# Kernel tuning notes

Hardware: AMD Instinct MI355X
Metric: run time of the kernel (lower is better)

## Reference

```python
import jax, jax.numpy as jnp
import numpy as np

N_NODES = 100000
N_EDGES = 3200000
D_IN = 256
D_OUT = 128


def setup_inputs() -> dict:
    key = jax.random.key(0)
    k1, k2, k3, k4, k5 = jax.random.split(key, 5)
    x = jax.random.normal(k1, (N_NODES, D_IN), dtype=jnp.float32)
    edge_src = jax.random.randint(k2, (N_EDGES,), 0, N_NODES, dtype=jnp.int32)
    edge_dst = jax.random.randint(k3, (N_EDGES,), 0, N_NODES, dtype=jnp.int32)
    edge_weight = jax.random.uniform(k4, (N_EDGES,), dtype=jnp.float32)
    # GraphConvolution weight init: uniform(-stdv, stdv), stdv = 1/sqrt(in+out)
    stdv = 1.0 / np.sqrt(D_IN + D_OUT)
    W = jax.random.uniform(k5, (D_IN, D_OUT), dtype=jnp.float32,
                           minval=-stdv, maxval=stdv)
    return {"x": x, "edge_src": edge_src, "edge_dst": edge_dst,
            "edge_weight": edge_weight, "W": W}


def reference(x, edge_src, edge_dst, edge_weight, W):
    # support = input @ weight  (dense GEMM)  [N, D_OUT]
    support = x @ W
    # out = spmm(adj, support): out[d] = sum_{e: dst(e)=d} w_e * support[src(e)]
    msgs = support[edge_src] * edge_weight[:, None]       # [E, D_OUT] gather
    out = jax.ops.segment_sum(msgs, edge_dst, num_segments=N_NODES)  # scatter-add
    return out
```

## Files before the change

kernel.cpp:

```cpp
#include <hip/hip_runtime.h>


#define DIN 256
#define DOUT 128
#define SB_SHIFT 10
#define SB_NODES 1024
#define MAX_NSB 128
#define TILE 4096
#define SPLIT 2

struct alignas(8) EdgeRec { int src; float w; };

typedef __attribute__((ext_vector_type(8))) short bf16x8;
typedef __attribute__((ext_vector_type(4))) float f32x4;

__device__ __forceinline__ unsigned pack_bf16x2(float a, float b) {
  unsigned ua = __float_as_uint(a);
  unsigned ub = __float_as_uint(b);
  ua += 0x7fffu + ((ua >> 16) & 1u);
  ub += 0x7fffu + ((ub >> 16) & 1u);
  return (ua >> 16) | (ub & 0xffff0000u);
}
__device__ __forceinline__ unsigned short bf16_rne(float a) {
  unsigned ua = __float_as_uint(a);
  ua += 0x7fffu + ((ua >> 16) & 1u);
  return (unsigned short)(ua >> 16);
}
__device__ __forceinline__ float bf_lo(unsigned p) { return __uint_as_float(p << 16); }
__device__ __forceinline__ float bf_hi(unsigned p) { return __uint_as_float(p & 0xffff0000u); }

__global__ __launch_bounds__(256) void wtrans_kernel(const float* __restrict__ W,
                                                     unsigned short* __restrict__ Wt) {
  __shared__ float s[64][65];
  int t = threadIdx.x;
  int kt = blockIdx.x >> 1;
  int nt = blockIdx.x & 1;
#pragma unroll
  for (int i = 0; i < 16; i++) {
    int idx = i * 256 + t;
    int kk = idx >> 6, nn = idx & 63;
    s[kk][nn] = W[(size_t)(kt * 64 + kk) * DOUT + nt * 64 + nn];
  }
  __syncthreads();
#pragma unroll
  for (int i = 0; i < 16; i++) {
    int idx = i * 256 + t;
    int nn = idx >> 6, kk = idx & 63;
    Wt[(size_t)(nt * 64 + nn) * DIN + kt * 64 + kk] = bf16_rne(s[kk][nn]);
  }
}

__global__ __launch_bounds__(256) void gemm_mfma_kernel(const float* __restrict__ x,
                                                        const unsigned short* __restrict__ Wt,
                                                        unsigned short* __restrict__ support,
                                                        int M) {
  const int lane = threadIdx.x & 63;
  const int wave = threadIdx.x >> 6;
  const int wr = wave >> 1, wc = wave & 1;
  const int m = lane & 15, kg = lane >> 4;
  const int rowBase = blockIdx.x * 128 + wr * 64;

  f32x4 acc[4][4];
#pragma unroll
  for (int rt = 0; rt < 4; rt++)
#pragma unroll
    for (int ct = 0; ct < 4; ct++) acc[rt][ct] = (f32x4)(0.f);

  const float* arow[4];
#pragma unroll
  for (int rt = 0; rt < 4; rt++) {
    int r = rowBase + rt * 16 + m;
    if (r > M - 1) r = M - 1;
    arow[rt] = x + (size_t)r * DIN + kg * 8;
  }
  const unsigned short* brow[4];
#pragma unroll
  for (int ct = 0; ct < 4; ct++)
    brow[ct] = Wt + (size_t)(wc * 64 + ct * 16 + m) * DIN + kg * 8;

#pragma unroll 2
  for (int k0 = 0; k0 < DIN; k0 += 32) {
    bf16x8 af[4], bfr[4];
#pragma unroll
    for (int rt = 0; rt < 4; rt++) {
      float4 a0 = *(const float4*)(arow[rt] + k0);
      float4 a1 = *(const float4*)(arow[rt] + k0 + 4);
      union { bf16x8 f; unsigned u[4]; } ua;
      ua.u[0] = pack_bf16x2(a0.x, a0.y);
      ua.u[1] = pack_bf16x2(a0.z, a0.w);
      ua.u[2] = pack_bf16x2(a1.x, a1.y);
      ua.u[3] = pack_bf16x2(a1.z, a1.w);
      af[rt] = ua.f;
    }
#pragma unroll
    for (int ct = 0; ct < 4; ct++) {
      union { bf16x8 f; uint4 u; } ub;
      ub.u = *(const uint4*)(brow[ct] + k0);
      bfr[ct] = ub.f;
    }
#pragma unroll
    for (int rt = 0; rt < 4; rt++)
#pragma unroll
      for (int ct = 0; ct < 4; ct++)
        acc[rt][ct] = __builtin_amdgcn_mfma_f32_16x16x32_bf16(af[rt], bfr[ct],
                                                              acc[rt][ct], 0, 0, 0);
  }

#pragma unroll
  for (int rt = 0; rt < 4; rt++) {
#pragma unroll
    for (int r = 0; r < 4; r++) {
      int row = rowBase + rt * 16 + kg * 4 + r;
      if (row < M) {
#pragma unroll
        for (int ct = 0; ct < 4; ct++) {
          int col = wc * 64 + ct * 16 + m;
          support[(size_t)row * DOUT + col] = bf16_rne(acc[rt][ct][r]);
        }
      }
    }
  }
}

__global__ __launch_bounds__(256) void sbhist_kernel(const int* __restrict__ dst, int E,
                                                     int nsb, int* __restrict__ sb_tot) {
  __shared__ int h[MAX_NSB];
  int t = threadIdx.x;
  for (int i = t; i < nsb; i += 256) h[i] = 0;
  __syncthreads();
  int e4 = E >> 2;
  for (int i = blockIdx.x * 256 + t; i < e4; i += gridDim.x * 256) {
    int4 d = *(const int4*)&dst[i * 4];
    atomicAdd(&h[d.x >> SB_SHIFT], 1);
    atomicAdd(&h[d.y >> SB_SHIFT], 1);
    atomicAdd(&h[d.z >> SB_SHIFT], 1);
    atomicAdd(&h[d.w >> SB_SHIFT], 1);
  }
  if (blockIdx.x == 0 && t < (E & 3)) atomicAdd(&h[dst[e4 * 4 + t] >> SB_SHIFT], 1);
  __syncthreads();
  for (int i = t; i < nsb; i += 256)
    if (h[i]) atomicAdd(&sb_tot[i], h[i]);
}

__global__ __launch_bounds__(128) void sbscan_kernel(const int* __restrict__ sb_tot, int nsb,
                                                     int* __restrict__ sb_base,
                                                     int* __restrict__ sb_cur) {
  __shared__ int s[128];
  int t = threadIdx.x;
  int v = (t < nsb) ? sb_tot[t] : 0;
  s[t] = v;
  __syncthreads();
  for (int off = 1; off < 128; off <<= 1) {
    int u = (t >= off) ? s[t - off] : 0;
    __syncthreads();
    s[t] += u;
    __syncthreads();
  }
  if (t < nsb) {
    int excl = s[t] - v;
    sb_base[t] = excl;
    sb_cur[t] = excl;
  }
}

__global__ __launch_bounds__(256) void bin1_kernel(const int* __restrict__ src,
                                                   const int* __restrict__ dst,
                                                   const float* __restrict__ w,
                                                   int E, int nsb,
                                                   int* __restrict__ sb_cur,
                                                   uint2* __restrict__ bin) {
  __shared__ uint2 recs[TILE];
  __shared__ unsigned short sbid[TILE];
  __shared__ int hist[MAX_NSB], segstart[MAX_NSB], cursor[MAX_NSB], sbbase[MAX_NSB];
  __shared__ int sc[128];
  int t = threadIdx.x;
  int e0 = blockIdx.x * TILE;
  int cnt = min(TILE, E - e0);

  for (int i = t; i < nsb; i += 256) hist[i] = 0;
  __syncthreads();
  for (int k = 0; k < TILE / 256; k++) {
    int e = e0 + k * 256 + t;
    if (e < E) atomicAdd(&hist[dst[e] >> SB_SHIFT], 1);
  }
  __syncthreads();
  if (t < 128) sc[t] = (t < nsb) ? hist[t] : 0;
  __syncthreads();
  for (int off = 1; off < 128; off <<= 1) {
    int v = 0;
    if (t < 128 && t >= off) v = sc[t - off];
    __syncthreads();
    if (t < 128) sc[t] += v;
    __syncthreads();
  }
  if (t < nsb) {
    int c = hist[t];
    int excl = sc[t] - c;
    segstart[t] = excl;
    cursor[t] = excl;
    if (c > 0) sbbase[t] = atomicAdd(&sb_cur[t], c);
  }
  __syncthreads();
  for (int k = 0; k < TILE / 256; k++) {
    int e = e0 + k * 256 + t;
    if (e < E) {
      int d = dst[e];
      int sb = d >> SB_SHIFT;
      int slot = atomicAdd(&cursor[sb], 1);
      recs[slot] = make_uint2((unsigned)src[e] | ((unsigned)(d & (SB_NODES - 1)) << 17),
                              __float_as_uint(w[e]));
      sbid[slot] = (unsigned short)sb;
    }
  }
  __syncthreads();
  for (int k = 0; k < TILE / 256; k++) {
    int slot = k * 256 + t;
    if (slot < cnt) {
      int sb = sbid[slot];
      bin[sbbase[sb] + (slot - segstart[sb])] = recs[slot];
    }
  }
}

__global__ __launch_bounds__(256) void bin2_kernel(const uint2* __restrict__ bin,
                                                   const int* __restrict__ sb_base,
                                                   const int* __restrict__ sb_cur,
                                                   int N, int E,
                                                   int* __restrict__ row_ptr,
                                                   EdgeRec* __restrict__ csr) {
  __shared__ int lhist[SB_NODES];
  __shared__ int part[256];
  int t = threadIdx.x;
  int sb = blockIdx.x / SPLIT;
  int q = blockIdx.x % SPLIT;
  int nodeBase = sb * SB_NODES;
  int beg = sb_base[sb];
  int end = sb_cur[sb];

  for (int i = t; i < SB_NODES; i += 256) lhist[i] = 0;
  __syncthreads();
  for (int i = beg + t; i < end; i += 256) {
    uint2 r = bin[i];
    atomicAdd(&lhist[(r.x >> 17) & (SB_NODES - 1)], 1);
  }
  __syncthreads();
  int a0 = lhist[4 * t], a1 = lhist[4 * t + 1], a2 = lhist[4 * t + 2], a3 = lhist[4 * t + 3];
  int tsum = a0 + a1 + a2 + a3;
  part[t] = tsum;
  __syncthreads();
  for (int off = 1; off < 256; off <<= 1) {
    int v = (t >= off) ? part[t - off] : 0;
    __syncthreads();
    part[t] += v;
    __syncthreads();
  }
  int excl = part[t] - tsum;
  lhist[4 * t] = excl;
  lhist[4 * t + 1] = excl + a0;
  lhist[4 * t + 2] = excl + a0 + a1;
  lhist[4 * t + 3] = excl + a0 + a1 + a2;
  __syncthreads();
  if (q == 0) {
    for (int l = t; l < SB_NODES; l += 256) {
      int node = nodeBase + l;
      if (node < N) row_ptr[node] = beg + lhist[l];
    }
    if (t == 0 && nodeBase + SB_NODES >= N) row_ptr[N] = E;
  }
  __syncthreads();
  int lo = q * (SB_NODES / SPLIT);
  int hi = lo + (SB_NODES / SPLIT);
  for (int i = beg + t; i < end; i += 256) {
    uint2 r = bin[i];
    int local = (int)((r.x >> 17) & (SB_NODES - 1));
    if (local >= lo && local < hi) {
      int pos = beg + atomicAdd(&lhist[local], 1);
      EdgeRec er;
      er.src = (int)(r.x & 0x1FFFFu);
      er.w = __uint_as_float(r.y);
      csr[pos] = er;
    }
  }
}

__global__ __launch_bounds__(256) void spmm_kernel(const unsigned* __restrict__ sup,
                                                   const int* __restrict__ row_ptr,
                                                   const EdgeRec* __restrict__ csr,
                                                   float* __restrict__ out, int N) {
  int wave = threadIdx.x >> 6;
  int lane = threadIdx.x & 63;
  int node = blockIdx.x * 4 + wave;
  if (node >= N) return;
  int j0 = row_ptr[node];
  int j1 = row_ptr[node + 1];
  float accx = 0.f, accy = 0.f;
  for (int base = j0; base < j1; base += 64) {
    int cnt = min(64, j1 - base);
    int mysrc = 0, myw = 0;
    if (lane < cnt) {
      EdgeRec r = csr[base + lane];
      mysrc = r.src;
      myw = __float_as_int(r.w);
    }
    int j = 0;
    for (; j + 8 <= cnt; j += 8) {
      int s[8]; float w[8]; unsigned p[8];
#pragma unroll
      for (int u = 0; u < 8; u++) {
        s[u] = __builtin_amdgcn_readlane(mysrc, j + u);
        w[u] = __int_as_float(__builtin_amdgcn_readlane(myw, j + u));
      }
#pragma unroll
      for (int u = 0; u < 8; u++) p[u] = sup[(size_t)s[u] * 64 + lane];
#pragma unroll
      for (int u = 0; u < 8; u++) {
        accx += w[u] * bf_lo(p[u]);
        accy += w[u] * bf_hi(p[u]);
      }
    }
    for (; j < cnt; j++) {
      int sj = __builtin_amdgcn_readlane(mysrc, j);
      float wj = __int_as_float(__builtin_amdgcn_readlane(myw, j));
      unsigned pj = sup[(size_t)sj * 64 + lane];
      accx += wj * bf_lo(pj);
      accy += wj * bf_hi(pj);
    }
  }
  ((float2*)out)[(size_t)node * 64 + lane] = make_float2(accx, accy);
}

__global__ void scatter_kernel(const float* __restrict__ x, const float* __restrict__ W,
                               const int* __restrict__ src, const int* __restrict__ dst,
                               const float* __restrict__ w, long long total,
                               float* __restrict__ out) {
  long long i = (long long)blockIdx.x * blockDim.x + threadIdx.x;
  if (i < total) {
    int e = (int)(i >> 7);
    int c = (int)(i & 127);
    float acc = 0.f;
    const float* xr = &x[(size_t)src[e] * DIN];
    for (int k = 0; k < DIN; k++) acc += xr[k] * W[(size_t)k * DOUT + c];
    atomicAdd(&out[(size_t)dst[e] * DOUT + c], w[e] * acc);
  }
}

extern "C" void kernel_launch(void* const* d_in, const int* in_sizes, int n_in,
                              void* d_out, int out_size, void* d_ws, size_t ws_size,
                              hipStream_t stream) {
  const float* x = (const float*)d_in[0];
  const int* esrc = (const int*)d_in[1];
  const int* edst = (const int*)d_in[2];
  const float* ew = (const float*)d_in[3];
  const float* W = (const float*)d_in[4];
  float* out = (float*)d_out;

  const int N = in_sizes[0] / DIN;
  const int E = in_sizes[1];
  const int nsb = (N + SB_NODES - 1) / SB_NODES;

  char* ws = (char*)d_ws;
  size_t off = 0;
  auto alloc = [&](size_t bytes) {
    size_t o = off;
    off = (off + bytes + 255) & ~(size_t)255;
    return o;
  };
  size_t sup_off = alloc((size_t)N * DOUT * 2);
  size_t wt_off = alloc((size_t)DOUT * DIN * 2);
  size_t rp_off = alloc((size_t)(N + 1) * 4);
  size_t sbt_off = alloc(MAX_NSB * 4);
  size_t sbb_off = alloc(MAX_NSB * 4);
  size_t sbc_off = alloc(MAX_NSB * 4);
  size_t bin_off = alloc((size_t)E * 8);
  size_t csr_off = alloc((size_t)E * 8);
  bool use_csr = (off <= ws_size);

  unsigned short* support = (unsigned short*)(ws + sup_off);
  unsigned short* Wt = (unsigned short*)(ws + wt_off);
  int* row_ptr = (int*)(ws + rp_off);
  int* sb_tot = (int*)(ws + sbt_off);
  int* sb_base = (int*)(ws + sbb_off);
  int* sb_cur = (int*)(ws + sbc_off);
  uint2* bin = (uint2*)(ws + bin_off);
  EdgeRec* csr = (EdgeRec*)(ws + csr_off);

  if (use_csr) {
    wtrans_kernel<<<8, 256, 0, stream>>>(W, Wt);
    gemm_mfma_kernel<<<(N + 127) / 128, 256, 0, stream>>>(x, Wt, support, N);
    hipMemsetAsync(sb_tot, 0, MAX_NSB * 4, stream);
    sbhist_kernel<<<512, 256, 0, stream>>>(edst, E, nsb, sb_tot);
    sbscan_kernel<<<1, 128, 0, stream>>>(sb_tot, nsb, sb_base, sb_cur);
    bin1_kernel<<<(E + TILE - 1) / TILE, 256, 0, stream>>>(esrc, edst, ew, E, nsb,
                                                           sb_cur, bin);
    bin2_kernel<<<nsb * SPLIT, 256, 0, stream>>>(bin, sb_base, sb_cur, N, E,
                                                 row_ptr, csr);
    spmm_kernel<<<(N + 3) / 4, 256, 0, stream>>>((const unsigned*)support, row_ptr, csr,
                                                 out, N);
  } else {
    hipMemsetAsync(out, 0, (size_t)N * DOUT * 4, stream);
    long long total = (long long)E * DOUT;
    scatter_kernel<<<(int)((total + 255) / 256), 256, 0, stream>>>(x, W, esrc, edst, ew,
                                                                   total, out);
  }
}
```

Measured before the change: 486.8 us.

## Vectorize SpMM gathers to 16-byte loads across 4 edge groups; retile GEMM waves

The SpMM kernel now splits each wave into four 16-lane groups. Each group handles a different edge and loads a full 256-byte bf16 support row with 16-byte vector loads, replacing per-lane 4-byte loads. Partial sums from the groups are combined with cross-lane shuffles and written as float4. The GEMM kernel is retiled so each wave computes 32 rows by all 128 columns instead of 64x64, changing register use and B-operand reuse. Trade-offs are padded, zero-weighted edge slots when a node's degree is not a multiple of 16, plus the shuffle reduction cost.

```diff
diff --git a/kernel.cpp b/kernel.cpp
--- a/kernel.cpp
+++ b/kernel.cpp
@@ -56,33 +56,32 @@
                                                         int M) {
   const int lane = threadIdx.x & 63;
   const int wave = threadIdx.x >> 6;
-  const int wr = wave >> 1, wc = wave & 1;
   const int m = lane & 15, kg = lane >> 4;
-  const int rowBase = blockIdx.x * 128 + wr * 64;
-
-  f32x4 acc[4][4];
-#pragma unroll
-  for (int rt = 0; rt < 4; rt++)
-#pragma unroll
-    for (int ct = 0; ct < 4; ct++) acc[rt][ct] = (f32x4)(0.f);
-
-  const float* arow[4];
-#pragma unroll
-  for (int rt = 0; rt < 4; rt++) {
+  const int rowBase = blockIdx.x * 128 + wave * 32;
+
+  f32x4 acc[2][8];
+#pragma unroll
+  for (int rt = 0; rt < 2; rt++)
+#pragma unroll
+    for (int ct = 0; ct < 8; ct++) acc[rt][ct] = (f32x4)(0.f);
+
+  const float* arow[2];
+#pragma unroll
+  for (int rt = 0; rt < 2; rt++) {
     int r = rowBase + rt * 16 + m;
     if (r > M - 1) r = M - 1;
     arow[rt] = x + (size_t)r * DIN + kg * 8;
   }
-  const unsigned short* brow[4];
-#pragma unroll
-  for (int ct = 0; ct < 4; ct++)
-    brow[ct] = Wt + (size_t)(wc * 64 + ct * 16 + m) * DIN + kg * 8;
+  const unsigned short* brow[8];
+#pragma unroll
+  for (int ct = 0; ct < 8; ct++)
+    brow[ct] = Wt + (size_t)(ct * 16 + m) * DIN + kg * 8;
 
 #pragma unroll 2
   for (int k0 = 0; k0 < DIN; k0 += 32) {
-    bf16x8 af[4], bfr[4];
-#pragma unroll
-    for (int rt = 0; rt < 4; rt++) {
+    bf16x8 af[2], bfr[8];
+#pragma unroll
+    for (int rt = 0; rt < 2; rt++) {
       float4 a0 = *(const float4*)(arow[rt] + k0);
       float4 a1 = *(const float4*)(arow[rt] + k0 + 4);
       union { bf16x8 f; unsigned u[4]; } ua;
@@ -93,28 +92,28 @@
       af[rt] = ua.f;
     }
 #pragma unroll
-    for (int ct = 0; ct < 4; ct++) {
+    for (int ct = 0; ct < 8; ct++) {
       union { bf16x8 f; uint4 u; } ub;
       ub.u = *(const uint4*)(brow[ct] + k0);
       bfr[ct] = ub.f;
     }
 #pragma unroll
-    for (int rt = 0; rt < 4; rt++)
-#pragma unroll
-      for (int ct = 0; ct < 4; ct++)
+    for (int rt = 0; rt < 2; rt++)
+#pragma unroll
+      for (int ct = 0; ct < 8; ct++)
         acc[rt][ct] = __builtin_amdgcn_mfma_f32_16x16x32_bf16(af[rt], bfr[ct],
                                                               acc[rt][ct], 0, 0, 0);
   }
 
 #pragma unroll
-  for (int rt = 0; rt < 4; rt++) {
+  for (int rt = 0; rt < 2; rt++) {
 #pragma unroll
     for (int r = 0; r < 4; r++) {
       int row = rowBase + rt * 16 + kg * 4 + r;
       if (row < M) {
 #pragma unroll
-        for (int ct = 0; ct < 4; ct++) {
-          int col = wc * 64 + ct * 16 + m;
+        for (int ct = 0; ct < 8; ct++) {
+          int col = ct * 16 + m;
           support[(size_t)row * DOUT + col] = bf16_rne(acc[rt][ct][r]);
         }
       }
@@ -289,44 +288,61 @@
                                                    float* __restrict__ out, int N) {
   int wave = threadIdx.x >> 6;
   int lane = threadIdx.x & 63;
+  int g = lane >> 4;
+  int c = lane & 15;
   int node = blockIdx.x * 4 + wave;
   if (node >= N) return;
   int j0 = row_ptr[node];
   int j1 = row_ptr[node + 1];
-  float accx = 0.f, accy = 0.f;
+  float acc[8];
+#pragma unroll
+  for (int i = 0; i < 8; i++) acc[i] = 0.f;
+
   for (int base = j0; base < j1; base += 64) {
     int cnt = min(64, j1 - base);
-    int mysrc = 0, myw = 0;
+    int mysrc = 0;
+    float myw = 0.f;
     if (lane < cnt) {
       EdgeRec r = csr[base + lane];
       mysrc = r.src;
-      myw = __float_as_int(r.w);
-    }
-    int j = 0;
-    for (; j + 8 <= cnt; j += 8) {
-      int s[8]; float w[8]; unsigned p[8];
-#pragma unroll
-      for (int u = 0; u < 8; u++) {
-        s[u] = __builtin_amdgcn_readlane(mysrc, j + u);
-        w[u] = __int_as_float(__builtin_amdgcn_readlane(myw, j + u));
+      myw = r.w;
+    }
+    for (int j = 0; j < cnt; j += 16) {
+      uint4 p[4];
+      float wv[4];
+#pragma unroll
+      for (int u = 0; u < 4; u++) {
+        int e = j + 4 * u + g;
+        int jj = min(e, cnt - 1);
+        int s = __shfl(mysrc, jj, 64);
+        float ww = __shfl(myw, jj, 64);
+        wv[u] = (e < cnt) ? ww : 0.f;
+        p[u] = *(const uint4*)(sup + (size_t)s * 64 + c * 4);
       }
 #pragma unroll
-      for (int u = 0; u < 8; u++) p[u] = sup[(size_t)s[u] * 64 + lane];
-#pragma unroll
-      for (int u = 0; u < 8; u++) {
-        accx += w[u] * bf_lo(p[u]);
-        accy += w[u] * bf_hi(p[u]);
+      for (int u = 0; u < 4; u++) {
+        unsigned pv0 = p[u].x, pv1 = p[u].y, pv2 = p[u].z, pv3 = p[u].w;
+        acc[0] += wv[u] * bf_lo(pv0);
+        acc[1] += wv[u] * bf_hi(pv0);
+        acc[2] += wv[u] * bf_lo(pv1);
+        acc[3] += wv[u] * bf_hi(pv1);
+        acc[4] += wv[u] * bf_lo(pv2);
+        acc[5] += wv[u] * bf_hi(pv2);
+        acc[6] += wv[u] * bf_lo(pv3);
+        acc[7] += wv[u] * bf_hi(pv3);
       }
     }
-    for (; j < cnt; j++) {
-      int sj = __builtin_amdgcn_readlane(mysrc, j);
-      float wj = __int_as_float(__builtin_amdgcn_readlane(myw, j));
-      unsigned pj = sup[(size_t)sj * 64 + lane];
-      accx += wj * bf_lo(pj);
-      accy += wj * bf_hi(pj);
-    }
-  }
-  ((float2*)out)[(size_t)node * 64 + lane] = make_float2(accx, accy);
+  }
+#pragma unroll
+  for (int i = 0; i < 8; i++) {
+    acc[i] += __shfl_xor(acc[i], 16, 64);
+    acc[i] += __shfl_xor(acc[i], 32, 64);
+  }
+  if (g == 0) {
+    float* orow = out + (size_t)node * DOUT + c * 8;
+    *(float4*)orow = make_float4(acc[0], acc[1], acc[2], acc[3]);
+    *(float4*)(orow + 4) = make_float4(acc[4], acc[5], acc[6], acc[7]);
+  }
 }
 
 __global__ void scatter_kernel(const float* __restrict__ x, const float* __restrict__ W,
```

Result: no change. 485.5 us (-0.3%).
